# Kernel optimization log

Hardware: AMD Instinct MI355X
Metric: run time of the kernel (lower is better)

Reference implementation:

```python
import jax, jax.numpy as jnp
import numpy as np

ALPHA = 2.0   # spikingjelly surrogate.ATan default alpha
TAU = 2.0
VTH = 1.0
EPS = 1e-5

@jax.custom_vjp
def atan_spike(x):
    return (x >= 0.0).astype(x.dtype)

def _as_fwd(x):
    return atan_spike(x), x

def _as_bwd(x, g):
    # ATan surrogate derivative: alpha/2 / (1 + (pi/2*alpha*x)^2)
    return (g * (ALPHA / 2.0) / (1.0 + (jnp.pi / 2.0 * ALPHA * x) ** 2),)

atan_spike.defvjp(_as_fwd, _as_bwd)

def lif_multistep(x):
    # x: [B, T, D]; LIF with decay_input=True, v_reset=0 (hard reset), detach_reset=True
    xt = jnp.swapaxes(x, 0, 1)  # [T, B, D] time-major
    def step(v, xi):
        v = v + (xi - v) / TAU                       # integrate with input decay
        s = atan_spike(v - VTH)                       # fire (surrogate grad)
        v = v * (1.0 - jax.lax.stop_gradient(s))      # hard reset to 0, detached
        return v, s
    _, spikes = jax.lax.scan(step, jnp.zeros_like(xt[0]), xt)
    return jnp.swapaxes(spikes, 0, 1)  # [B, T, D]

def layernorm(x, g, b):
    m = x.mean(-1, keepdims=True)
    v = x.var(-1, keepdims=True)
    return (x - m) / jnp.sqrt(v + EPS) * g + b

def setup_inputs() -> dict:
    key = jax.random.key(0)
    ks = jax.random.split(key, 6)
    B, T, IN, HP, E, H, D = 256, 256, 4, 64, 512, 1024, 4
    s = 0.02
    return {
        "hist_feat": jax.random.normal(ks[0], (B, T, IN), jnp.float32),
        "pW1": jax.random.normal(ks[1], (IN, HP), jnp.float32) * s,
        "pb1": jnp.zeros((HP,), jnp.float32),
        "pW2": jax.random.normal(ks[2], (HP, E), jnp.float32) * s,
        "pb2": jnp.zeros((E,), jnp.float32),
        "fc1_w": jax.random.normal(ks[3], (D, E, H), jnp.float32) * s,
        "fc1_b": jnp.zeros((D, H), jnp.float32),
        "ln1_g": jnp.ones((D, H), jnp.float32),
        "ln1_b": jnp.zeros((D, H), jnp.float32),
        "fc2_w": jax.random.normal(ks[4], (D, H, E), jnp.float32) * s,
        "fc2_b": jnp.zeros((D, E), jnp.float32),
        "ln2_g": jnp.ones((D, E), jnp.float32),
        "ln2_b": jnp.zeros((D, E), jnp.float32),
    }

def reference(hist_feat, pW1, pb1, pW2, pb2, fc1_w, fc1_b, ln1_g, ln1_b,
              fc2_w, fc2_b, ln2_g, ln2_b):
    # input projector: Linear -> exact GELU -> Linear
    x = jax.nn.gelu(hist_feat @ pW1 + pb1, approximate=False) @ pW2 + pb2  # [B,T,E]
    depth = fc1_w.shape[0]
    for d in range(depth):  # small fixed layer loop
        res = x
        h = layernorm(x @ fc1_w[d] + fc1_b[d], ln1_g[d], ln1_b[d])  # [B,T,H]
        h = lif_multistep(h)
        h = layernorm(h @ fc2_w[d] + fc2_b[d], ln2_g[d], ln2_b[d])  # [B,T,E]
        h = lif_multistep(h)
        x = res + h  # dropout is identity in eval mode
    return x[:, -1]  # pooling='last', no mask -> last timestep, [B,E]
```

## Files before the change

kernel.cpp:

```cpp
#include <hip/hip_runtime.h>
#include <hip/hip_bf16.h>
#include <math.h>

#define B_  256
#define T_  256
#define IN_ 4
#define HP_ 64
#define E_  512
#define H_  1024
#define D_  4

typedef __hip_bfloat16 bf16;
typedef _Float16 f16;
typedef _Float16 f16x8 __attribute__((ext_vector_type(8)));
typedef float f32x4 __attribute__((ext_vector_type(4)));

__device__ __forceinline__ float load1(const void* p, size_t idx, bool isb) {
    if (isb) {
        unsigned int u = ((const unsigned short*)p)[idx];
        return __uint_as_float(u << 16);
    }
    return ((const float*)p)[idx];
}

__device__ __forceinline__ float4 load4(const void* p, size_t idx, bool isb) {
    if (isb) {
        ushort4 u = *(const ushort4*)((const unsigned short*)p + idx);
        float4 r;
        r.x = __uint_as_float(((unsigned int)u.x) << 16);
        r.y = __uint_as_float(((unsigned int)u.y) << 16);
        r.z = __uint_as_float(((unsigned int)u.z) << 16);
        r.w = __uint_as_float(((unsigned int)u.w) << 16);
        return r;
    }
    return *((const float4*)p + (idx >> 2));
}

__device__ __forceinline__ void split3(float x, f16& h, f16& hs, f16& lb) {
    h = (f16)x;
    float hf = (float)h;
    hs = (f16)(hf * 4.8828125e-4f);
    lb = (f16)((x - hf) * 2048.0f);
}

__global__ void sniff_count_kernel(const unsigned short* __restrict__ p,
                                   int* __restrict__ cnts) {
    __shared__ int cnt;
    if (threadIdx.x == 0) cnt = 0;
    __syncthreads();
    int local = 0;
    #pragma unroll
    for (int k = 0; k < 4; ++k) {
        int i = blockIdx.x * 1024 + k * 256 + threadIdx.x;
        unsigned int bits = ((unsigned int)p[i]) << 16;
        float v = __uint_as_float(bits);
        float a = fabsf(v);
        if (!(a <= 1e4f)) local++;
        else if (v != 0.0f && a < 1e-6f) local++;
    }
    atomicAdd(&cnt, local);
    __syncthreads();
    if (threadIdx.x == 0) cnts[blockIdx.x] = cnt;
}

__global__ void sniff_final_kernel(const int* __restrict__ cnts,
                                   int* __restrict__ flag) {
    int s = 0;
    for (int i = 0; i < 64; ++i) s += cnts[i];
    *flag = (s > 1024) ? 0 : 1;
}

__global__ __launch_bounds__(256) void wsplit_kernel(
        const void* __restrict__ W, size_t wOff, unsigned short* __restrict__ Wt,
        int K, int N, const int* __restrict__ flag) {
    const bool isb = (*flag != 0);
    __shared__ float tile[32][33];
    const int n0 = blockIdx.x * 32, k0 = blockIdx.y * 32;
    const int t = threadIdx.x;
    {
        int lk = t >> 3, ln0 = (t & 7) << 2;
        float4 v = load4(W, wOff + (size_t)(k0 + lk) * N + n0 + ln0, isb);
        tile[lk][ln0 + 0] = v.x; tile[lk][ln0 + 1] = v.y;
        tile[lk][ln0 + 2] = v.z; tile[lk][ln0 + 3] = v.w;
    }
    __syncthreads();
    int n = t >> 3, kq0 = (t & 7) << 2;
    size_t base = (size_t)(n0 + n) * (2 * (size_t)K) + k0 + kq0;
    #pragma unroll
    for (int j = 0; j < 4; ++j) {
        float x = tile[kq0 + j][n];
        f16 h, hs, lb;
        split3(x, h, hs, lb);
        Wt[base + j]     = *(unsigned short*)&h;
        Wt[base + j + K] = *(unsigned short*)&lb;
    }
}

template<int NPL>
__device__ __forceinline__ void gemm_mfma_body(
        const unsigned short* __restrict__ At, const unsigned short* __restrict__ Wt,
        const void* __restrict__ bias, size_t bOff,
        float* __restrict__ C, int N, int K, const int* __restrict__ flag) {
    const bool isb = (*flag != 0);
    constexpr int APL = (NPL == 3) ? 2 : 1;
    __shared__ unsigned short As[128 * 64];
    __shared__ unsigned short Bs[128 * 64];

    const int gx = N >> 7;
    const int gy = (int)gridDim.x / gx;
    int bx, by;
    {
        int bid = blockIdx.x;
        if ((gy & 7) == 0) {
            int k = bid & 7, i = bid >> 3;
            bx = i % gx;
            by = (gy >> 3) * k + i / gx;
        } else { bx = bid % gx; by = bid / gx; }
    }
    const int bn = bx * 128;
    const int bm = by * 128;

    const int tid  = threadIdx.x;
    const int lane = tid & 63;
    const int wave = tid >> 6;
    const int wm = wave >> 1;
    const int wn = wave & 1;
    const int g  = lane >> 4;
    const int lr = lane & 15;

    const int sar = tid >> 1;
    const int sah = tid & 1;
    const int sbn = tid >> 1;
    const int sq  = tid & 1;

    const f16 C11 = (f16)4.8828125e-4f;
    const f16x8 c11v = {C11, C11, C11, C11, C11, C11, C11, C11};

    f32x4 acc[4][4];
    #pragma unroll
    for (int i = 0; i < 4; ++i)
        #pragma unroll
        for (int j = 0; j < 4; ++j) acc[i][j] = (f32x4){0.f, 0.f, 0.f, 0.f};

    const unsigned short* Ap = At + (size_t)(bm + sar) * (APL * (size_t)K) + sah * 16;
    const unsigned short* Wp = Wt + (size_t)(bn + sbn) * (2 * (size_t)K) + sq * 16;

    f16x8 av[2 * APL], wv[4];
    #pragma unroll
    for (int pl = 0; pl < APL; ++pl)
        #pragma unroll
        for (int c = 0; c < 2; ++c)
            av[pl * 2 + c] = *(const f16x8*)(Ap + (size_t)pl * K + c * 8);
    #pragma unroll
    for (int pl = 0; pl < 2; ++pl)
        #pragma unroll
        for (int c = 0; c < 2; ++c)
            wv[pl * 2 + c] = *(const f16x8*)(Wp + (size_t)pl * K + c * 8);

    const int nt = K >> 5;
    for (int t = 0; t < nt; ++t) {
        const int arb = sar * 64, asw = sar & 7;
        #pragma unroll
        for (int pl = 0; pl < APL; ++pl)
            #pragma unroll
            for (int c = 0; c < 2; ++c) {
                const int gg = sah * 2 + c;
                *(f16x8*)&As[arb + (((pl << 2) | gg) ^ asw) * 8] = av[pl * 2 + c];
            }
        const int brb = sbn * 64, bsw = sbn & 7;
        #pragma unroll
        for (int pl = 0; pl < 2; ++pl)
            #pragma unroll
            for (int c = 0; c < 2; ++c) {
                const int gg = sq * 2 + c;
                *(f16x8*)&Bs[brb + (((pl << 2) | gg) ^ bsw) * 8] = wv[pl * 2 + c];
            }
        __syncthreads();
        if (t + 1 < nt) {
            const int k0 = (t + 1) << 5;
            #pragma unroll
            for (int pl = 0; pl < APL; ++pl)
                #pragma unroll
                for (int c = 0; c < 2; ++c)
                    av[pl * 2 + c] = *(const f16x8*)(Ap + (size_t)pl * K + k0 + c * 8);
            #pragma unroll
            for (int pl = 0; pl < 2; ++pl)
                #pragma unroll
                for (int c = 0; c < 2; ++c)
                    wv[pl * 2 + c] = *(const f16x8*)(Wp + (size_t)pl * K + k0 + c * 8);
        }
        f16x8 a0[4], b0[4], b2[4], a2[4];
        #pragma unroll
        for (int mi = 0; mi < 4; ++mi) {
            const int ar = wm * 64 + mi * 16 + lr;
            a0[mi] = *(const f16x8*)&As[ar * 64 + ((g ^ (ar & 7))) * 8];
            if (NPL == 3)
                a2[mi] = *(const f16x8*)&As[ar * 64 + (((4 | g) ^ (ar & 7))) * 8];
        }
        #pragma unroll
        for (int ni = 0; ni < 4; ++ni) {
            const int br = wn * 64 + ni * 16 + lr;
            b0[ni] = *(const f16x8*)&Bs[br * 64 + ((g ^ (br & 7))) * 8];
            b2[ni] = *(const f16x8*)&Bs[br * 64 + (((4 | g) ^ (br & 7))) * 8];
        }
        #pragma unroll
        for (int mi = 0; mi < 4; ++mi)
            #pragma unroll
            for (int ni = 0; ni < 4; ++ni)
                acc[mi][ni] = __builtin_amdgcn_mfma_f32_16x16x32_f16(
                    a0[mi], b0[ni], acc[mi][ni], 0, 0, 0);
        {
            f16x8 a1[4];
            #pragma unroll
            for (int mi = 0; mi < 4; ++mi) a1[mi] = a0[mi] * c11v;
            #pragma unroll
            for (int mi = 0; mi < 4; ++mi)
                #pragma unroll
                for (int ni = 0; ni < 4; ++ni)
                    acc[mi][ni] = __builtin_amdgcn_mfma_f32_16x16x32_f16(
                        a1[mi], b2[ni], acc[mi][ni], 0, 0, 0);
        }
        if (NPL == 3) {
            f16x8 b1[4];
            #pragma unroll
            for (int ni = 0; ni < 4; ++ni) b1[ni] = b0[ni] * c11v;
            #pragma unroll
            for (int mi = 0; mi < 4; ++mi)
                #pragma unroll
                for (int ni = 0; ni < 4; ++ni)
                    acc[mi][ni] = __builtin_amdgcn_mfma_f32_16x16x32_f16(
                        a2[mi], b1[ni], acc[mi][ni], 0, 0, 0);
        }
        __syncthreads();
    }
    #pragma unroll
    for (int ni = 0; ni < 4; ++ni) {
        const int col = bn + wn * 64 + ni * 16 + lr;
        const float bv = load1(bias, bOff + col, isb);
        #pragma unroll
        for (int mi = 0; mi < 4; ++mi) {
            #pragma unroll
            for (int r = 0; r < 4; ++r) {
                const size_t row = (size_t)(bm + wm * 64 + mi * 16 + g * 4 + r);
                C[row * N + col] = acc[mi][ni][r] + bv;
            }
        }
    }
}

__global__ __launch_bounds__(256, 3) void gemm_mfma3_kernel(
        const unsigned short* __restrict__ At, const unsigned short* __restrict__ Wt,
        const void* __restrict__ bias, size_t bOff,
        float* __restrict__ C, int N, int K, const int* __restrict__ flag) {
    gemm_mfma_body<3>(At, Wt, bias, bOff, C, N, K, flag);
}

__global__ __launch_bounds__(256, 3) void gemm_mfma2_kernel(
        const unsigned short* __restrict__ At, const unsigned short* __restrict__ Wt,
        const void* __restrict__ bias, size_t bOff,
        float* __restrict__ C, int N, int K, const int* __restrict__ flag) {
    gemm_mfma_body<2>(At, Wt, bias, bOff, C, N, K, flag);
}

#define RB_ 16
__global__ __launch_bounds__(256) void proj_kernel(
        const void* __restrict__ hist, const void* __restrict__ pW1,
        const void* __restrict__ pb1,  const void* __restrict__ pW2,
        const void* __restrict__ pb2,  float* __restrict__ Xc,
        unsigned short* __restrict__ At1,
        size_t m0, const int* __restrict__ flag) {
    const bool isb = (*flag != 0);
    __shared__ float h1[RB_][HP_];
    const size_t mb = (size_t)blockIdx.x * RB_;
    const int tid = threadIdx.x;
    const int lane = tid & 63;
    const int grp = tid >> 6;
    #pragma unroll
    for (int rep = 0; rep < 4; ++rep) {
        int idx = tid + rep * 256;
        int r = idx >> 6, c = idx & 63;
        size_t gm = m0 + mb + r;
        float acc = 0.f;
        #pragma unroll
        for (int i = 0; i < IN_; ++i)
            acc = fmaf(load1(hist, gm * IN_ + i, isb),
                       load1(pW1, (size_t)i * HP_ + c, isb), acc);
        acc += load1(pb1, c, isb);
        h1[r][c] = 0.5f * acc * (1.0f + erff(acc * 0.70710678118654752440f));
    }
    __syncthreads();
    const int e0 = lane * 8;
    float acc[4][8];
    #pragma unroll
    for (int r = 0; r < 4; ++r)
        #pragma unroll
        for (int j = 0; j < 8; ++j) acc[r][j] = 0.f;
    for (int i = 0; i < HP_; ++i) {
        float4 wA = load4(pW2, (size_t)i * E_ + e0, isb);
        float4 wB = load4(pW2, (size_t)i * E_ + e0 + 4, isb);
        float w[8] = {wA.x, wA.y, wA.z, wA.w, wB.x, wB.y, wB.z, wB.w};
        #pragma unroll
        for (int r = 0; r < 4; ++r) {
            float h = h1[grp * 4 + r][i];
            #pragma unroll
            for (int j = 0; j < 8; ++j) acc[r][j] = fmaf(h, w[j], acc[r][j]);
        }
    }
    #pragma unroll
    for (int r = 0; r < 4; ++r) {
        size_t row = mb + grp * 4 + r;
        float o[8];
        #pragma unroll
        for (int j = 0; j < 8; ++j)
            o[j] = acc[r][j] + load1(pb2, e0 + j, isb);
        *(float4*)(Xc + row * E_ + e0)     = (float4){o[0], o[1], o[2], o[3]};
        *(float4*)(Xc + row * E_ + e0 + 4) = (float4){o[4], o[5], o[6], o[7]};
        f16x8 hv, lv;
        #pragma unroll
        for (int j = 0; j < 8; ++j) {
            f16 h, hs, lb;
            split3(o[j], h, hs, lb);
            hv[j] = h; lv[j] = lb;
        }
        *(f16x8*)&At1[row * (2 * E_) + e0]      = hv;
        *(f16x8*)&At1[row * (2 * E_) + E_ + e0] = lv;
    }
}

__device__ __forceinline__ float block_sum(float v, float* smem, int tid) {
    #pragma unroll
    for (int off = 32; off > 0; off >>= 1) v += __shfl_down(v, off, 64);
    __syncthreads();
    if ((tid & 63) == 0) smem[tid >> 6] = v;
    __syncthreads();
    if (tid == 0) smem[4] = smem[0] + smem[1] + smem[2] + smem[3];
    __syncthreads();
    return smem[4];
}

__global__ __launch_bounds__(256) void ln_stats_kernel(const float* __restrict__ Y,
                                                       float* __restrict__ stats,
                                                       int N) {
    __shared__ float smem[5];
    size_t row = blockIdx.x;
    const float* y = Y + row * (size_t)N;
    int tid = threadIdx.x;
    int nPer = N >> 8;
    float vals[4];
    float s = 0.f;
    for (int i = 0; i < nPer; ++i) { float v = y[tid + (i << 8)]; vals[i] = v; s += v; }
    float mean = block_sum(s, smem, tid) / (float)N;
    float sq = 0.f;
    for (int i = 0; i < nPer; ++i) { float d0 = vals[i] - mean; sq += d0 * d0; }
    float var = block_sum(sq, smem, tid) / (float)N;
    if (tid == 0) {
        stats[row * 2]     = mean;
        stats[row * 2 + 1] = sqrtf(var + 1e-5f);
    }
}

__global__ __launch_bounds__(64) void lif_kernel(const float* __restrict__ Y,
                                                 const float* __restrict__ stats,
                                                 const void* __restrict__ g, size_t gOff,
                                                 const void* __restrict__ b, size_t bOff,
                                                 unsigned short* __restrict__ At2,
                                                 int N, const int* __restrict__ flag) {
    const bool isb = (*flag != 0);
    int f = blockIdx.x * 64 + threadIdx.x;
    int bb = blockIdx.y;
    const float gw = load1(g, gOff + f, isb);
    const float bw = load1(b, bOff + f, isb);
    size_t base = (size_t)bb * T_ * N + f;
    size_t srow = (size_t)bb * T_;
    float v = 0.f;
    for (int t0 = 0; t0 < T_; t0 += 8) {
        float x[8], mn[8], dn[8], s[8];
        #pragma unroll
        for (int j = 0; j < 8; ++j) {
            x[j]  = Y[base + (size_t)(t0 + j) * N];
            mn[j] = stats[(srow + t0 + j) * 2];
            dn[j] = stats[(srow + t0 + j) * 2 + 1];
        }
        #pragma unroll
        for (int j = 0; j < 8; ++j) {
            float xn = (x[j] - mn[j]) / dn[j] * gw + bw;
            v = v + (xn - v) * 0.5f;
            s[j] = (v - 1.0f >= 0.0f) ? 1.0f : 0.0f;
            v = v * (1.0f - s[j]);
        }
        #pragma unroll
        for (int j = 0; j < 8; ++j) {
            f16 h = (f16)s[j];
            At2[base + (size_t)(t0 + j) * N] = *(unsigned short*)&h;
        }
    }
}

__global__ __launch_bounds__(64) void lif_add_kernel(const float* __restrict__ Z,
                                                     const float* __restrict__ stats,
                                                     const void* __restrict__ g, size_t gOff,
                                                     const void* __restrict__ b, size_t bOff,
                                                     float* __restrict__ Xc,
                                                     unsigned short* __restrict__ At1,
                                                     const int* __restrict__ flag) {
    const bool isb = (*flag != 0);
    int e = blockIdx.x * 64 + threadIdx.x;
    int bb = blockIdx.y;
    const float gw = load1(g, gOff + e, isb);
    const float bw = load1(b, bOff + e, isb);
    size_t base  = (size_t)bb * T_ * E_ + e;
    size_t base2 = (size_t)bb * T_ * (2 * E_) + e;
    size_t srow  = (size_t)bb * T_;
    float v = 0.f;
    for (int t0 = 0; t0 < T_; t0 += 8) {
        float x[8], xc[8], mn[8], dn[8], s[8];
        #pragma unroll
        for (int j = 0; j < 8; ++j) {
            x[j]  = Z[base + (size_t)(t0 + j) * E_];
            mn[j] = stats[(srow + t0 + j) * 2];
            dn[j] = stats[(srow + t0 + j) * 2 + 1];
        }
        #pragma unroll
        for (int j = 0; j < 8; ++j) xc[j] = Xc[base + (size_t)(t0 + j) * E_];
        #pragma unroll
        for (int j = 0; j < 8; ++j) {
            float xn = (x[j] - mn[j]) / dn[j] * gw + bw;
            v = v + (xn - v) * 0.5f;
            s[j] = (v - 1.0f >= 0.0f) ? 1.0f : 0.0f;
            v = v * (1.0f - s[j]);
        }
        #pragma unroll
        for (int j = 0; j < 8; ++j) {
            float nx = xc[j] + s[j];
            Xc[base + (size_t)(t0 + j) * E_] = nx;
            f16 h, hs, lb;
            split3(nx, h, hs, lb);
            At1[base2 + (size_t)(t0 + j) * (2 * E_)]      = *(unsigned short*)&h;
            At1[base2 + (size_t)(t0 + j) * (2 * E_) + E_] = *(unsigned short*)&lb;
        }
    }
}

__global__ void out_kernel(const float* __restrict__ Xc, void* __restrict__ out,
                           int b0, const int* __restrict__ flag) {
    int i = blockIdx.x * 256 + threadIdx.x;
    int bl = i / E_, e = i - bl * E_;
    float v = Xc[((size_t)bl * T_ + (T_ - 1)) * E_ + e];
    size_t oi = (size_t)(b0 + bl) * E_ + e;
    if (*flag) ((bf16*)out)[oi] = __float2bfloat16(v);
    else       ((float*)out)[oi] = v;
}

extern "C" void kernel_launch(void* const* d_in, const int* in_sizes, int n_in,
                              void* d_out, int out_size, void* d_ws, size_t ws_size,
                              hipStream_t stream) {
    char* ws = (char*)d_ws;
    int* flag = (int*)ws;
    int* cnts = (int*)(ws + 64);

    const size_t wtCount = 2 * (size_t)E_ * H_;
    const size_t wtBytes = 2 * D_ * wtCount * sizeof(unsigned short);
    unsigned short* Wt1 = (unsigned short*)(ws + 512);
    unsigned short* Wt2 = Wt1 + (size_t)D_ * wtCount;

    size_t used = 512 + wtBytes;
    size_t avail = (ws_size > used) ? ws_size - used : 0;
    const size_t perBatch = (size_t)T_ * ((E_ + H_ + E_) * 4 + 2 * E_ * 2 + H_ * 2 + 16);
    int CB = 256;
    while (CB > 1 && (size_t)CB * perBatch > avail) CB >>= 1;
    const int R = CB * T_;

    float* Xc  = (float*)(ws + used);
    float* HBc = Xc + (size_t)R * E_;
    float* Y2c = HBc + (size_t)R * H_;
    unsigned short* At1 = (unsigned short*)(Y2c + (size_t)R * E_);
    unsigned short* At2 = At1 + (size_t)R * 2 * E_;
    float* St1 = (float*)(At2 + (size_t)R * H_);
    float* St2 = St1 + (size_t)R * 2;

    sniff_count_kernel<<<64, 256, 0, stream>>>((const unsigned short*)d_in[0], cnts);
    sniff_final_kernel<<<1, 1, 0, stream>>>(cnts, flag);

    for (int d = 0; d < D_; ++d) {
        wsplit_kernel<<<dim3(H_ / 32, E_ / 32), 256, 0, stream>>>(
            d_in[5], (size_t)d * E_ * H_, Wt1 + (size_t)d * wtCount, E_, H_, flag);
        wsplit_kernel<<<dim3(E_ / 32, H_ / 32), 256, 0, stream>>>(
            d_in[9], (size_t)d * H_ * E_, Wt2 + (size_t)d * wtCount, H_, E_, flag);
    }

    for (int b0 = 0; b0 < B_; b0 += CB) {
        proj_kernel<<<R / RB_, 256, 0, stream>>>(d_in[0], d_in[1], d_in[2], d_in[3],
                                                 d_in[4], Xc, At1, (size_t)b0 * T_, flag);
        for (int d = 0; d < D_; ++d) {
            size_t b1o = (size_t)d * H_;
            size_t b2o = (size_t)d * E_;

            gemm_mfma3_kernel<<<(H_ / 128) * (R / 128), 256, 0, stream>>>(
                At1, Wt1 + (size_t)d * wtCount, d_in[6], b1o, HBc, H_, E_, flag);
            ln_stats_kernel<<<R, 256, 0, stream>>>(HBc, St1, H_);
            lif_kernel<<<dim3(H_ / 64, CB), 64, 0, stream>>>(
                HBc, St1, d_in[7], b1o, d_in[8], b1o, At2, H_, flag);

            gemm_mfma2_kernel<<<(E_ / 128) * (R / 128), 256, 0, stream>>>(
                At2, Wt2 + (size_t)d * wtCount, d_in[10], b2o, Y2c, E_, H_, flag);
            ln_stats_kernel<<<R, 256, 0, stream>>>(Y2c, St2, E_);
            lif_add_kernel<<<dim3(E_ / 64, CB), 64, 0, stream>>>(
                Y2c, St2, d_in[11], b2o, d_in[12], b2o, Xc, At1, flag);
        }
        out_kernel<<<(CB * E_) / 256, 256, 0, stream>>>(Xc, d_out, b0, flag);
    }
}
```

Baseline: 3.414 ms.

## Double-buffer GEMM shared tiles, unroll LIF loops deeper, fuse output write into LIF

Shared-memory A/B tiles in the MFMA GEMM are double-buffered, which removes the trailing barrier in each K iteration. The LIF and LIF-add kernels now process 16 timesteps per unrolled chunk instead of 8, putting more loads in flight. The separate output kernel is folded into the last layer's lif_add kernel, saving one launch. The doubled shared memory (64KB per block) may reduce occupancy below the launch-bounds target of 3 blocks per CU.

```diff
diff --git a/kernel.cpp b/kernel.cpp
--- a/kernel.cpp
+++ b/kernel.cpp
@@ -103,8 +103,8 @@
         float* __restrict__ C, int N, int K, const int* __restrict__ flag) {
     const bool isb = (*flag != 0);
     constexpr int APL = (NPL == 3) ? 2 : 1;
-    __shared__ unsigned short As[128 * 64];
-    __shared__ unsigned short Bs[128 * 64];
+    __shared__ unsigned short As[2][128 * 64];
+    __shared__ unsigned short Bs[2][128 * 64];
 
     const int gx = N >> 7;
     const int gy = (int)gridDim.x / gx;
@@ -159,13 +159,14 @@
 
     const int nt = K >> 5;
     for (int t = 0; t < nt; ++t) {
+        const int cur = t & 1;
         const int arb = sar * 64, asw = sar & 7;
         #pragma unroll
         for (int pl = 0; pl < APL; ++pl)
             #pragma unroll
             for (int c = 0; c < 2; ++c) {
                 const int gg = sah * 2 + c;
-                *(f16x8*)&As[arb + (((pl << 2) | gg) ^ asw) * 8] = av[pl * 2 + c];
+                *(f16x8*)&As[cur][arb + (((pl << 2) | gg) ^ asw) * 8] = av[pl * 2 + c];
             }
         const int brb = sbn * 64, bsw = sbn & 7;
         #pragma unroll
@@ -173,7 +174,7 @@
             #pragma unroll
             for (int c = 0; c < 2; ++c) {
                 const int gg = sq * 2 + c;
-                *(f16x8*)&Bs[brb + (((pl << 2) | gg) ^ bsw) * 8] = wv[pl * 2 + c];
+                *(f16x8*)&Bs[cur][brb + (((pl << 2) | gg) ^ bsw) * 8] = wv[pl * 2 + c];
             }
         __syncthreads();
         if (t + 1 < nt) {
@@ -193,15 +194,15 @@
         #pragma unroll
         for (int mi = 0; mi < 4; ++mi) {
             const int ar = wm * 64 + mi * 16 + lr;
-            a0[mi] = *(const f16x8*)&As[ar * 64 + ((g ^ (ar & 7))) * 8];
+            a0[mi] = *(const f16x8*)&As[cur][ar * 64 + ((g ^ (ar & 7))) * 8];
             if (NPL == 3)
-                a2[mi] = *(const f16x8*)&As[ar * 64 + (((4 | g) ^ (ar & 7))) * 8];
+                a2[mi] = *(const f16x8*)&As[cur][ar * 64 + (((4 | g) ^ (ar & 7))) * 8];
         }
         #pragma unroll
         for (int ni = 0; ni < 4; ++ni) {
             const int br = wn * 64 + ni * 16 + lr;
-            b0[ni] = *(const f16x8*)&Bs[br * 64 + ((g ^ (br & 7))) * 8];
-            b2[ni] = *(const f16x8*)&Bs[br * 64 + (((4 | g) ^ (br & 7))) * 8];
+            b0[ni] = *(const f16x8*)&Bs[cur][br * 64 + ((g ^ (br & 7))) * 8];
+            b2[ni] = *(const f16x8*)&Bs[cur][br * 64 + (((4 | g) ^ (br & 7))) * 8];
         }
         #pragma unroll
         for (int mi = 0; mi < 4; ++mi)
@@ -231,7 +232,6 @@
                     acc[mi][ni] = __builtin_amdgcn_mfma_f32_16x16x32_f16(
                         a2[mi], b1[ni], acc[mi][ni], 0, 0, 0);
         }
-        __syncthreads();
     }
     #pragma unroll
     for (int ni = 0; ni < 4; ++ni) {
@@ -373,23 +373,23 @@
     size_t base = (size_t)bb * T_ * N + f;
     size_t srow = (size_t)bb * T_;
     float v = 0.f;
-    for (int t0 = 0; t0 < T_; t0 += 8) {
-        float x[8], mn[8], dn[8], s[8];
-        #pragma unroll
-        for (int j = 0; j < 8; ++j) {
+    for (int t0 = 0; t0 < T_; t0 += 16) {
+        float x[16], mn[16], dn[16], s[16];
+        #pragma unroll
+        for (int j = 0; j < 16; ++j) {
             x[j]  = Y[base + (size_t)(t0 + j) * N];
             mn[j] = stats[(srow + t0 + j) * 2];
             dn[j] = stats[(srow + t0 + j) * 2 + 1];
         }
         #pragma unroll
-        for (int j = 0; j < 8; ++j) {
+        for (int j = 0; j < 16; ++j) {
             float xn = (x[j] - mn[j]) / dn[j] * gw + bw;
             v = v + (xn - v) * 0.5f;
             s[j] = (v - 1.0f >= 0.0f) ? 1.0f : 0.0f;
             v = v * (1.0f - s[j]);
         }
         #pragma unroll
-        for (int j = 0; j < 8; ++j) {
+        for (int j = 0; j < 16; ++j) {
             f16 h = (f16)s[j];
             At2[base + (size_t)(t0 + j) * N] = *(unsigned short*)&h;
         }
@@ -402,6 +402,8 @@
                                                      const void* __restrict__ b, size_t bOff,
                                                      float* __restrict__ Xc,
                                                      unsigned short* __restrict__ At1,
+                                                     void* __restrict__ outp, int b0,
+                                                     int lastLayer,
                                                      const int* __restrict__ flag) {
     const bool isb = (*flag != 0);
     int e = blockIdx.x * 64 + threadIdx.x;
@@ -412,25 +414,25 @@
     size_t base2 = (size_t)bb * T_ * (2 * E_) + e;
     size_t srow  = (size_t)bb * T_;
     float v = 0.f;
-    for (int t0 = 0; t0 < T_; t0 += 8) {
-        float x[8], xc[8], mn[8], dn[8], s[8];
-        #pragma unroll
-        for (int j = 0; j < 8; ++j) {
+    for (int t0 = 0; t0 < T_; t0 += 16) {
+        float x[16], xc[16], mn[16], dn[16], s[16];
+        #pragma unroll
+        for (int j = 0; j < 16; ++j) {
             x[j]  = Z[base + (size_t)(t0 + j) * E_];
             mn[j] = stats[(srow + t0 + j) * 2];
             dn[j] = stats[(srow + t0 + j) * 2 + 1];
         }
         #pragma unroll
-        for (int j = 0; j < 8; ++j) xc[j] = Xc[base + (size_t)(t0 + j) * E_];
-        #pragma unroll
-        for (int j = 0; j < 8; ++j) {
+        for (int j = 0; j < 16; ++j) xc[j] = Xc[base + (size_t)(t0 + j) * E_];
+        #pragma unroll
+        for (int j = 0; j < 16; ++j) {
             float xn = (x[j] - mn[j]) / dn[j] * gw + bw;
             v = v + (xn - v) * 0.5f;
             s[j] = (v - 1.0f >= 0.0f) ? 1.0f : 0.0f;
             v = v * (1.0f - s[j]);
         }
         #pragma unroll
-        for (int j = 0; j < 8; ++j) {
+        for (int j = 0; j < 16; ++j) {
             float nx = xc[j] + s[j];
             Xc[base + (size_t)(t0 + j) * E_] = nx;
             f16 h, hs, lb;
@@ -438,17 +440,13 @@
             At1[base2 + (size_t)(t0 + j) * (2 * E_)]      = *(unsigned short*)&h;
             At1[base2 + (size_t)(t0 + j) * (2 * E_) + E_] = *(unsigned short*)&lb;
         }
-    }
-}
-
-__global__ void out_kernel(const float* __restrict__ Xc, void* __restrict__ out,
-                           int b0, const int* __restrict__ flag) {
-    int i = blockIdx.x * 256 + threadIdx.x;
-    int bl = i / E_, e = i - bl * E_;
-    float v = Xc[((size_t)bl * T_ + (T_ - 1)) * E_ + e];
-    size_t oi = (size_t)(b0 + bl) * E_ + e;
-    if (*flag) ((bf16*)out)[oi] = __float2bfloat16(v);
-    else       ((float*)out)[oi] = v;
+        if (lastLayer && t0 + 16 == T_) {
+            float nx = Xc[base + (size_t)(T_ - 1) * E_];
+            size_t oi = (size_t)(b0 + bb) * E_ + e;
+            if (isb) ((bf16*)outp)[oi] = __float2bfloat16(nx);
+            else     ((float*)outp)[oi] = nx;
+        }
+    }
 }
 
 extern "C" void kernel_launch(void* const* d_in, const int* in_sizes, int n_in,
@@ -505,8 +503,8 @@
                 At2, Wt2 + (size_t)d * wtCount, d_in[10], b2o, Y2c, E_, H_, flag);
             ln_stats_kernel<<<R, 256, 0, stream>>>(Y2c, St2, E_);
             lif_add_kernel<<<dim3(E_ / 64, CB), 64, 0, stream>>>(
-                Y2c, St2, d_in[11], b2o, d_in[12], b2o, Xc, At1, flag);
-        }
-        out_kernel<<<(CB * E_) / 256, 256, 0, stream>>>(Xc, d_out, b0, flag);
-    }
-}
+                Y2c, St2, d_in[11], b2o, d_in[12], b2o, Xc, At1,
+                d_out, b0, (d == D_ - 1) ? 1 : 0, flag);
+        }
+    }
+}
```

New measurement: 3.354 ms. About the same (-1.8%).
